# Kernel optimization log

Hardware: AMD Instinct MI355X
Metric: run time of the kernel (lower is better)

Reference implementation:

```python
import jax, jax.numpy as jnp
import numpy as np

WIN = 5
EPS = 1e-05


def box_sum(x, win=WIN):
    """3D box-filter window sum, SAME padding (pad=win//2), via separable 1D convs.
    Mathematically identical to F.conv3d(x, ones(1,1,win,win,win), padding=win//2).
    x: [N, C, D, H, W]
    """
    pad = win // 2
    for ax in range(3):  # D, H, W
        kshape = [1, 1, 1, 1, 1]
        kshape[2 + ax] = win
        k = jnp.ones(kshape, x.dtype)
        pads = [(0, 0), (0, 0), (0, 0)]
        pads[ax] = (pad, pad)
        x = jax.lax.conv_general_dilated(
            x, k, window_strides=(1, 1, 1), padding=pads,
            dimension_numbers=('NCDHW', 'OIDHW', 'NCDHW'))
    return x


def setup_inputs() -> dict:
    key = jax.random.key(0)
    k1, k2 = jax.random.split(key)
    shape = (2, 1, 160, 192, 192)
    I = jax.random.normal(k1, shape, dtype=jnp.float32)
    J = jax.random.normal(k2, shape, dtype=jnp.float32)
    return {"I": I, "J": J}


def reference(I, J):
    V = float(WIN ** 3)  # window voxel count
    I_sum = box_sum(I)
    J_sum = box_sum(J)
    I2_sum = box_sum(I * I)
    J2_sum = box_sum(J * J)
    IJ_sum = box_sum(I * J)

    u_I = I_sum / V
    u_J = J_sum / V
    cross = IJ_sum - u_J * I_sum - u_I * J_sum + u_I * u_J * V
    I_var = I2_sum - 2.0 * u_I * I_sum + u_I * u_I * V
    J_var = J2_sum - 2.0 * u_J * J_sum + u_J * u_J * V
    cc = cross * cross / (I_var * J_var + EPS)
    # single channel: avg over channels is identity; loss = -mean(cc)
    return -1.0 * jnp.mean(cc)
```

## Files before the change

### kernel.cpp

```cpp
#include <hip/hip_runtime.h>


namespace {
constexpr int Wd = 192, Hd = 192, Dd = 160;
constexpr int SH = 192;
constexpr int SD = 192 * 192;
constexpr long SN = (long)SD * Dd;
constexpr int CD = 6;
constexpr int NCHUNK = 27;
constexpr int TROW = 72;
constexpr int TILEF = 2 * 20 * TROW;
constexpr float INV_V = 1.0f / 125.0f;
constexpr float EPSf = 1e-5f;

__device__ __forceinline__ void wslide(const float h[8], float o[4]) {
  float s0 = h[0] + h[1] + h[2] + h[3] + h[4];
  float s1 = s0 - h[0] + h[5];
  float s2 = s1 - h[1] + h[6];
  float s3 = s2 - h[2] + h[7];
  o[0] = s0; o[1] = s1; o[2] = s2; o[3] = s3;
}

__device__ __forceinline__ void gl_lds16(const float* g, float* l) {
  __builtin_amdgcn_global_load_lds(
      (const __attribute__((address_space(1))) void*)g,
      (__attribute__((address_space(3))) void*)l, 16, 0, 0);
}
}

__global__ __launch_bounds__(256) void ncc_fused(const float* __restrict__ I,
                                                 const float* __restrict__ Jv,
                                                 float* __restrict__ out) {
  __shared__ float tile[3][TILEF];
  __shared__ float red[4];

  const int tid = threadIdx.x;
  const int tx = tid & 15;
  const int ty = tid >> 4;
  const int wbase = blockIdx.x * 64;
  const int hbase = blockIdx.y * 16;
  const int n  = blockIdx.z / NCHUNK;
  const int d_lo = (blockIdx.z % NCHUNK) * CD;

  const float* Ib = I  + (long)n * SN;
  const float* Jb = Jv + (long)n * SN;

  const int wave = tid >> 6, lane = tid & 63;
  const int arr = wave >> 1;
  const float* gsrc = arr ? Jb : Ib;
  int goff[3]; int loff[3]; bool on[3];
  #pragma unroll
  for (int r = 0; r < 3; ++r) {
    const int seg = wave * 180 + r * 64 + lane;
    on[r] = (r < 2) || (lane < 52);
    const int rem = seg - arr * 360;
    const int row = rem / 18, c16 = rem % 18;
    const int hh = hbase + row - 2;
    const int hc = min(max(hh, 0), Hd - 1);
    const int gw = wbase - 2 + c16 * 4;
    const int gc = min(max(gw, 0), Wd - 4);
    goff[r] = hc * SH + gc;
    loff[r] = seg * 4;
  }

  if (d_lo > 0) {
    const float* b0 = gsrc + (long)(d_lo - 2) * SD;
    const float* b1 = gsrc + (long)(d_lo - 1) * SD;
    #pragma unroll
    for (int r = 0; r < 3; ++r) if (on[r]) gl_lds16(b0 + goff[r], &tile[0][loff[r]]);
    #pragma unroll
    for (int r = 0; r < 3; ++r) if (on[r]) gl_lds16(b1 + goff[r], &tile[1][loff[r]]);
  }
  asm volatile("s_waitcnt vmcnt(0) lgkmcnt(0)" ::: "memory");
  __builtin_amdgcn_s_barrier();

  const bool fixl = (wbase == 0)   && (tx == 0);
  const bool fixr = (wbase == 128) && (tx == 15);

  float ring[5][5][4];
  float acc = 0.0f;

  int bc = 0;
  constexpr int T = CD + 4;
  for (int t0 = 0; t0 < T; t0 += 5) {
    #pragma unroll
    for (int p = 0; p < 5; ++p) {
      const int t = t0 + p;
      const int s = d_lo - 2 + t;

      const bool issue = ((t + 2) < T) && ((d_lo + t) < Dd);
      if (issue) {
        const float* base = gsrc + (long)(d_lo + t) * SD;
        int bw = bc - 1; if (bw < 0) bw += 3;
        float* dst = &tile[0][0] + bw * TILEF;
        #pragma unroll
        for (int r = 0; r < 3; ++r) if (on[r]) gl_lds16(base + goff[r], dst + loff[r]);
      }

      float hsI[8], hsJ[8], hsII[8], hsJJ[8], hsIJ[8];
      #pragma unroll
      for (int c = 0; c < 8; ++c) {
        hsI[c] = 0.f; hsJ[c] = 0.f; hsII[c] = 0.f; hsJJ[c] = 0.f; hsIJ[c] = 0.f;
      }
      if (s >= 0 && s < Dd) {
        const float* bufc = &tile[0][0] + bc * TILEF;
        #pragma unroll
        for (int dh = 0; dh < 5; ++dh) {
          const int rrow = ty + dh;
          const int hh = hbase + rrow - 2;
          if (hh >= 0 && hh < Hd) {
            const float* pa = bufc + rrow * TROW + 4 * tx;
            const float* pb = pa + 20 * TROW;
            float a[8], b[8];
            ((float4*)a)[0] = ((const float4*)pa)[0];
            ((float4*)a)[1] = ((const float4*)pa)[1];
            ((float4*)b)[0] = ((const float4*)pb)[0];
            ((float4*)b)[1] = ((const float4*)pb)[1];
            if (fixl) { a[2]=a[0]; a[3]=a[1]; a[0]=0.f; a[1]=0.f;
                        b[2]=b[0]; b[3]=b[1]; b[0]=0.f; b[1]=0.f; }
            if (fixr) { a[4]=a[6]; a[5]=a[7]; a[6]=0.f; a[7]=0.f;
                        b[4]=b[6]; b[5]=b[7]; b[6]=0.f; b[7]=0.f; }
            #pragma unroll
            for (int c = 0; c < 8; ++c) {
              const float x = a[c], y = b[c];
              hsI[c]  += x;
              hsJ[c]  += y;
              hsII[c] = fmaf(x, x, hsII[c]);
              hsJJ[c] = fmaf(y, y, hsJJ[c]);
              hsIJ[c] = fmaf(x, y, hsIJ[c]);
            }
          }
        }
      }

      wslide(hsI,  ring[p][0]);
      wslide(hsJ,  ring[p][1]);
      wslide(hsII, ring[p][2]);
      wslide(hsJJ, ring[p][3]);
      wslide(hsIJ, ring[p][4]);

      const int d = d_lo + t - 4;
      if (t >= 4 && d < Dd) {
        #pragma unroll
        for (int k = 0; k < 4; ++k) {
          float SI = 0.f, SJ = 0.f, SII = 0.f, SJJ = 0.f, SIJ = 0.f;
          #pragma unroll
          for (int q = 0; q < 5; ++q) {
            SI  += ring[q][0][k];
            SJ  += ring[q][1][k];
            SII += ring[q][2][k];
            SJJ += ring[q][3][k];
            SIJ += ring[q][4][k];
          }
          const float cross = SIJ - SI * SJ * INV_V;
          const float vI    = SII - SI * SI * INV_V;
          const float vJ    = SJJ - SJ * SJ * INV_V;
          acc += cross * cross / (vI * vJ + EPSf);
        }
      }

      if (issue) asm volatile("s_waitcnt vmcnt(3) lgkmcnt(0)" ::: "memory");
      else       asm volatile("s_waitcnt vmcnt(0) lgkmcnt(0)" ::: "memory");
      __builtin_amdgcn_s_barrier();
      bc += 1; if (bc == 3) bc = 0;
    }
  }

  #pragma unroll
  for (int off = 32; off > 0; off >>= 1) acc += __shfl_xor(acc, off, 64);
  if ((tid & 63) == 0) red[tid >> 6] = acc;
  __syncthreads();
  if (tid == 0) {
    const float total = red[0] + red[1] + red[2] + red[3];
    atomicAdd(out, total * (-1.0f / 11796480.0f));
  }
}

extern "C" void kernel_launch(void* const* d_in, const int* in_sizes, int n_in,
                              void* d_out, int out_size, void* d_ws, size_t ws_size,
                              hipStream_t stream) {
  const float* I = (const float*)d_in[0];
  const float* J = (const float*)d_in[1];
  float* out = (float*)d_out;
  hipMemsetAsync(out, 0, sizeof(float), stream);
  dim3 grid(3, 12, 2 * NCHUNK);
  ncc_fused<<<grid, 256, 0, stream>>>(I, J, out);
}
```

Measured before the change: 169.1 us.

## Give each wave a private LDS halo region to drop block-wide barriers

Each wave now loads its own 8-row halo (4 output rows plus the 4-row vertical halo) for both I and J into a private double-buffered LDS region. Previously the block shared a triple-buffered tile and had a barrier every depth step. Removing the cross-wave dependency drops the s_barrier, and launch bounds now request 4 blocks per CU. The cost is redundant halo loads: each wave fetches 8 rows for 4 outputs, which doubles global/L2 traffic. The prefetch distance also shrinks to one step with a full vmcnt(0) wait, giving less latency hiding per wave.

```diff
diff --git a/kernel.cpp b/kernel.cpp
--- a/kernel.cpp
+++ b/kernel.cpp
@@ -9,7 +9,9 @@
 constexpr int CD = 6;
 constexpr int NCHUNK = 27;
 constexpr int TROW = 72;
-constexpr int TILEF = 2 * 20 * TROW;
+constexpr int ARRF = 8 * TROW;
+constexpr int BUFF = 2 * ARRF;
+constexpr int WREGF = 2 * BUFF;
 constexpr float INV_V = 1.0f / 125.0f;
 constexpr float EPSf = 1e-5f;
 
@@ -28,51 +30,49 @@
 }
 }
 
-__global__ __launch_bounds__(256) void ncc_fused(const float* __restrict__ I,
-                                                 const float* __restrict__ Jv,
-                                                 float* __restrict__ out) {
-  __shared__ float tile[3][TILEF];
+__global__ __launch_bounds__(256, 4) void ncc_fused(const float* __restrict__ I,
+                                                    const float* __restrict__ Jv,
+                                                    float* __restrict__ out) {
+  __shared__ float tile[4 * WREGF];
   __shared__ float red[4];
 
-  const int tid = threadIdx.x;
-  const int tx = tid & 15;
-  const int ty = tid >> 4;
+  const int tid  = threadIdx.x;
+  const int lane = tid & 63, wave = tid >> 6;
+  const int tx   = lane & 15;
+  const int tyw  = lane >> 4;
   const int wbase = blockIdx.x * 64;
   const int hbase = blockIdx.y * 16;
-  const int n  = blockIdx.z / NCHUNK;
+  const int n   = blockIdx.z / NCHUNK;
   const int d_lo = (blockIdx.z % NCHUNK) * CD;
+  const int hw0 = hbase + 4 * wave - 2;
 
   const float* Ib = I  + (long)n * SN;
   const float* Jb = Jv + (long)n * SN;
+  const long  dJ  = (long)(Jb - Ib);
 
-  const int wave = tid >> 6, lane = tid & 63;
-  const int arr = wave >> 1;
-  const float* gsrc = arr ? Jb : Ib;
-  int goff[3]; int loff[3]; bool on[3];
+  long goffL[5]; int lloc[5]; bool on[5];
   #pragma unroll
-  for (int r = 0; r < 3; ++r) {
-    const int seg = wave * 180 + r * 64 + lane;
-    on[r] = (r < 2) || (lane < 52);
-    const int rem = seg - arr * 360;
+  for (int r = 0; r < 5; ++r) {
+    const int seg = r * 64 + lane;
+    on[r] = (r < 4) || (lane < 32);
+    const int arr = (seg >= 144) ? 1 : 0;
+    const int rem = seg - arr * 144;
     const int row = rem / 18, c16 = rem % 18;
-    const int hh = hbase + row - 2;
+    const int hh = hw0 + row;
     const int hc = min(max(hh, 0), Hd - 1);
     const int gw = wbase - 2 + c16 * 4;
     const int gc = min(max(gw, 0), Wd - 4);
-    goff[r] = hc * SH + gc;
-    loff[r] = seg * 4;
+    goffL[r] = (arr ? dJ : 0L) + (long)(hc * SH + gc);
+    lloc[r]  = seg * 4;
   }
+  float* wreg = &tile[wave * WREGF];
 
   if (d_lo > 0) {
-    const float* b0 = gsrc + (long)(d_lo - 2) * SD;
-    const float* b1 = gsrc + (long)(d_lo - 1) * SD;
+    const float* base = Ib + (long)(d_lo - 2) * SD;
     #pragma unroll
-    for (int r = 0; r < 3; ++r) if (on[r]) gl_lds16(b0 + goff[r], &tile[0][loff[r]]);
-    #pragma unroll
-    for (int r = 0; r < 3; ++r) if (on[r]) gl_lds16(b1 + goff[r], &tile[1][loff[r]]);
+    for (int r = 0; r < 5; ++r) if (on[r]) gl_lds16(base + goffL[r], wreg + lloc[r]);
   }
   asm volatile("s_waitcnt vmcnt(0) lgkmcnt(0)" ::: "memory");
-  __builtin_amdgcn_s_barrier();
 
   const bool fixl = (wbase == 0)   && (tx == 0);
   const bool fixr = (wbase == 128) && (tx == 15);
@@ -80,7 +80,7 @@
   float ring[5][5][4];
   float acc = 0.0f;
 
-  int bc = 0;
+  int bcur = 0;
   constexpr int T = CD + 4;
   for (int t0 = 0; t0 < T; t0 += 5) {
     #pragma unroll
@@ -88,13 +88,12 @@
       const int t = t0 + p;
       const int s = d_lo - 2 + t;
 
-      const bool issue = ((t + 2) < T) && ((d_lo + t) < Dd);
+      const bool issue = ((t + 1) < T) && ((s + 1) >= 0) && ((s + 1) < Dd);
       if (issue) {
-        const float* base = gsrc + (long)(d_lo + t) * SD;
-        int bw = bc - 1; if (bw < 0) bw += 3;
-        float* dst = &tile[0][0] + bw * TILEF;
+        const float* base = Ib + (long)(s + 1) * SD;
+        float* dst = wreg + (bcur ^ 1) * BUFF;
         #pragma unroll
-        for (int r = 0; r < 3; ++r) if (on[r]) gl_lds16(base + goff[r], dst + loff[r]);
+        for (int r = 0; r < 5; ++r) if (on[r]) gl_lds16(base + goffL[r], dst + lloc[r]);
       }
 
       float hsI[8], hsJ[8], hsII[8], hsJJ[8], hsIJ[8];
@@ -103,14 +102,14 @@
         hsI[c] = 0.f; hsJ[c] = 0.f; hsII[c] = 0.f; hsJJ[c] = 0.f; hsIJ[c] = 0.f;
       }
       if (s >= 0 && s < Dd) {
-        const float* bufc = &tile[0][0] + bc * TILEF;
+        const float* bufc = wreg + bcur * BUFF;
         #pragma unroll
         for (int dh = 0; dh < 5; ++dh) {
-          const int rrow = ty + dh;
-          const int hh = hbase + rrow - 2;
+          const int rrow = tyw + dh;
+          const int hh = hw0 + rrow;
           if (hh >= 0 && hh < Hd) {
             const float* pa = bufc + rrow * TROW + 4 * tx;
-            const float* pb = pa + 20 * TROW;
+            const float* pb = pa + ARRF;
             float a[8], b[8];
             ((float4*)a)[0] = ((const float4*)pa)[0];
             ((float4*)a)[1] = ((const float4*)pa)[1];
@@ -159,16 +158,14 @@
         }
       }
 
-      if (issue) asm volatile("s_waitcnt vmcnt(3) lgkmcnt(0)" ::: "memory");
-      else       asm volatile("s_waitcnt vmcnt(0) lgkmcnt(0)" ::: "memory");
-      __builtin_amdgcn_s_barrier();
-      bc += 1; if (bc == 3) bc = 0;
+      asm volatile("s_waitcnt vmcnt(0) lgkmcnt(0)" ::: "memory");
+      bcur ^= 1;
     }
   }
 
   #pragma unroll
   for (int off = 32; off > 0; off >>= 1) acc += __shfl_xor(acc, off, 64);
-  if ((tid & 63) == 0) red[tid >> 6] = acc;
+  if (lane == 0) red[wave] = acc;
   __syncthreads();
   if (tid == 0) {
     const float total = red[0] + red[1] + red[2] + red[3];
```

After: 541.5 us. +220.3%, slower.
